# Kernel tuning notes

Measured on AMD Instinct MI355X. Metric: run time of the kernel, lower is better.

Reference implementation:

```python
import jax, jax.numpy as jnp
import numpy as np
from jax import lax

B, D, K = 65536, 256, 32  # batch, num_latent_dims, flow_depth


def setup_inputs() -> dict:
    key = jax.random.key(0)
    k1, k2, k3, k4, k5 = jax.random.split(key, 5)
    X = jax.random.normal(k1, (B, D), dtype=jnp.float32)
    h = jax.random.normal(k2, (B, D), dtype=jnp.float32)  # passed through, unused by planar math
    u = jax.random.normal(k3, (K, D), dtype=jnp.float32) * 0.1
    w = jax.random.normal(k4, (K, D), dtype=jnp.float32) * 0.1
    b = jax.random.normal(k5, (K,), dtype=jnp.float32) * 0.1
    return {"X": X, "h": h, "u": u, "w": w, "b": b}


def _planar_chain(z0, u, w, b):
    """Sequential planar normalizing flow: z_{k+1} = z_k + u_hat_k * tanh(w_k.z_k + b_k)."""

    def step(z, params):
        u_k, w_k, b_k = params  # (D,), (D,), scalar
        # enforce invertibility: u_hat so that w.u_hat >= -1
        wu = jnp.dot(w_k, u_k)
        u_hat = u_k + (jax.nn.softplus(wu) - 1.0 - wu) * w_k / jnp.dot(w_k, w_k)
        lin = z @ w_k + b_k              # (B,)
        t = jnp.tanh(lin)                # (B,)
        z_new = z + t[:, None] * u_hat[None, :]
        # psi = (1 - t^2) w ; log|det J| = log|1 + psi.u_hat|
        log_det = jnp.log(jnp.abs(1.0 + (1.0 - t * t) * jnp.dot(w_k, u_hat)) + 1e-8)
        return z_new, log_det

    z_final, log_dets = lax.scan(step, z0, (u, w, b))
    return z_final, log_dets  # (B, D), (K, B)


def reference(X, h, u, w, b):
    z = X.reshape(X.shape[0], X.shape[1])  # view(B, D, -1) then view(B, D) -> (B, D)
    z_final, log_det_jacobians = _planar_chain(z, u, w, b)
    return z_final, log_det_jacobians
```

## Files before the change

### kernel.cpp

```cpp
#include <hip/hip_runtime.h>


#define B_ 65536
#define D_ 256
#define K_ 32

__device__ float g_ws[17472];

__global__ __launch_bounds__(256) void nf_pre(const float* __restrict__ u_in,
                                              const float* __restrict__ w_in,
                                              const float* __restrict__ b_in) {
  __shared__ float wls[32 * 257];
  __shared__ float red[256];
  __shared__ float dots[128];
  __shared__ float coefk_s;
  const int t = threadIdx.x;
  const int myk = blockIdx.x;

  {
    const float4* wp = (const float4*)w_in;
#pragma unroll
    for (int j = 0; j < 8; ++j) {
      int idx = j * 256 + t;
      float4 v = wp[idx];
      int e = idx * 4;
      int k = e >> 8, d = e & 255;
      wls[k * 257 + d]     = v.x;
      wls[k * 257 + d + 1] = v.y;
      wls[k * 257 + d + 2] = v.z;
      wls[k * 257 + d + 3] = v.w;
    }
  }
  __syncthreads();

  {
    int id = t & 127, hh = t >> 7;
    int j = id & 31, typ = id >> 5;
    const float* A;
    const float* Bp;
    if (typ == 0)      { A = u_in + j * 256; Bp = wls + j * 257; }
    else if (typ == 1) { A = wls + j * 257;  Bp = wls + j * 257; }
    else if (typ == 2) { A = wls + j * 257;  Bp = wls + myk * 257; }
    else               { A = u_in + j * 256; Bp = wls + myk * 257; }
    float acc = 0.f;
    int d0 = hh * 128;
#pragma unroll 8
    for (int d = 0; d < 128; ++d) acc = fmaf(A[d0 + d], Bp[d0 + d], acc);
    red[t] = acc;
  }
  __syncthreads();
  if (t < 128) dots[t] = red[t] + red[t + 128];
  __syncthreads();

  float* wT = g_ws;
  float* uhatT = g_ws + 8192;
  float* Gt = g_ws + 16384;
  float* cs = g_ws + 17408;
  float* bfs = g_ws + 17440;

  if (t < 32) {
    float wu = dots[t], ww = dots[32 + t], wkw = dots[64 + t], ukw = dots[96 + t];
    float sp = fmaxf(wu, 0.f) + log1pf(__expf(-fabsf(wu)));
    float coef = (sp - 1.f - wu) / ww;
    Gt[myk * 32 + t] = fmaf(coef, wkw, ukw);
    if (t == myk) {
      cs[myk] = sp - 1.f;
      bfs[myk] = b_in[myk];
      coefk_s = coef;
    }
  }
  __syncthreads();
  {
    float coefk = coefk_s;
    float wv = wls[myk * 257 + t];
    float uhv = fmaf(coefk, wv, u_in[myk * 256 + t]);
    wT[t * 32 + myk] = wv;
    uhatT[t * 32 + myk] = uhv;
  }
}

__global__ __launch_bounds__(256) void nf_main(const float* __restrict__ X,
                                               float* __restrict__ out) {
  __shared__ float Xt[64 * 129];
  __shared__ float tls[128 * 33];

  const int t = threadIdx.x;
  const int lane = t & 63;
  const int r = ((t >> 7) << 6) | lane;
  const int half = __builtin_amdgcn_readfirstlane((t >> 6) & 1);
  const int hb = half * 32;
  const int row0 = blockIdx.x * 128;
  const size_t grow = (size_t)(row0 + r);
  const int r_ld = t >> 1, q = t & 1;

  const float* __restrict__ wT = g_ws;
  const float* __restrict__ uhatT = g_ws + 8192;
  const float* __restrict__ Gt = g_ws + 16384;
  const float* __restrict__ cs = g_ws + 17408;
  const float* __restrict__ bfs = g_ws + 17440;

  float4 pf[8];

  auto load_stage = [&](int s) {
    const float4* xp = (const float4*)X + (size_t)(row0 + r_ld) * 64 + s * 16 + q * 8;
#pragma unroll
    for (int j = 0; j < 8; ++j) pf[j] = xp[j];
  };
  auto store_stage = [&]() {
#pragma unroll
    for (int j = 0; j < 8; ++j) {
      int c0 = q * 32 + j * 4;
      Xt[(c0 + 0) * 129 + r_ld] = pf[j].x;
      Xt[(c0 + 1) * 129 + r_ld] = pf[j].y;
      Xt[(c0 + 2) * 129 + r_ld] = pf[j].z;
      Xt[(c0 + 3) * 129 + r_ld] = pf[j].w;
    }
  };

  float p[32];
#pragma unroll
  for (int k = 0; k < 32; ++k) p[k] = 0.f;

  load_stage(0);
  for (int s = 0; s < 4; ++s) {
    store_stage();
    __syncthreads();
    if (s < 3) load_stage(s + 1);
#pragma unroll
    for (int c = 0; c < 32; ++c) {
      float xc = Xt[(hb + c) * 129 + r];
      const float* wp = wT + (s * 64 + hb + c) * 32;
#pragma unroll
      for (int k = 0; k < 32; ++k) p[k] = fmaf(xc, wp[k], p[k]);
    }
    __syncthreads();
  }

  float* plds = Xt;
  if (half == 0) {
#pragma unroll
    for (int k = 0; k < 32; ++k) plds[r * 33 + k] = p[k];
  }
  load_stage(0);
  __syncthreads();

  float tv[32];
  if (half == 1) {
    float pfull[32];
#pragma unroll
    for (int k = 0; k < 32; ++k) pfull[k] = p[k] + plds[r * 33 + k] + bfs[k];
#pragma unroll
    for (int k = 0; k < 32; ++k) {
      float la = pfull[k], lb = 0.f;
      const float* gp = Gt + k * 32;
#pragma unroll
      for (int j = 0; j + 1 < k; j += 2) {
        la = fmaf(tv[j], gp[j], la);
        lb = fmaf(tv[j + 1], gp[j + 1], lb);
      }
      if (k & 1) la = fmaf(tv[k - 1], gp[k - 1], la);
      float lin = la + lb;
      float e = __expf(2.f * lin);
      float tk = 1.f - 2.f / (e + 1.f);
      tv[k] = tk;
      tls[r * 33 + k] = tk;
      float val = fabsf(fmaf(1.f - tk * tk, cs[k], 1.f)) + 1e-8f;
      out[(size_t)B_ * D_ + (size_t)k * B_ + grow] = __logf(val);
    }
  }
  __syncthreads();
#pragma unroll
  for (int k = 0; k < 32; ++k) tv[k] = tls[r * 33 + k];

  for (int s = 0; s < 4; ++s) {
    store_stage();
    __syncthreads();
    if (s < 3) load_stage(s + 1);
    float4 ov[8];
#pragma unroll
    for (int c2 = 0; c2 < 8; ++c2) {
      float zz[4];
#pragma unroll
      for (int m = 0; m < 4; ++m) {
        int cl = hb + c2 * 4 + m;
        float z0 = Xt[cl * 129 + r];
        const float* up = uhatT + (s * 64 + cl) * 32;
#pragma unroll
        for (int k = 0; k < 32; ++k) z0 = fmaf(tv[k], up[k], z0);
        zz[m] = z0;
      }
      ov[c2] = make_float4(zz[0], zz[1], zz[2], zz[3]);
    }
    float4* op = (float4*)(out + grow * 256 + s * 64 + hb);
#pragma unroll
    for (int c2 = 0; c2 < 8; ++c2) op[c2] = ov[c2];
    __syncthreads();
  }
}

extern "C" void kernel_launch(void* const* d_in, const int* in_sizes, int n_in,
                              void* d_out, int out_size, void* d_ws, size_t ws_size,
                              hipStream_t stream) {
  const float* X = (const float*)d_in[0];
  const float* u = (const float*)d_in[2];
  const float* w = (const float*)d_in[3];
  const float* b = (const float*)d_in[4];
  float* out = (float*)d_out;

  nf_pre<<<32, 256, 0, stream>>>(u, w, b);
  nf_main<<<B_ / 128, 256, 0, stream>>>(X, out);
}
```

Measured before the change: 241.2 us.

## Fuse parameter precompute into main kernel and use register-tiled outer-product GEMMs

Removes the separate preprocessing kernel: each block now recomputes u_hat, the Gram-like matrix G and the softplus coefficients from u, w and b in shared memory, then processes 256 rows instead of 128. Both the X·W projection and the t·u_hat update become 4x8 register-tiled outer products reading float4 from LDS, replacing per-thread 32-wide scalar loops over global/constant data. The aim is to save a launch and serialization and to raise arithmetic intensity per LDS load. In exchange every block redundantly does the small O(K²D) setup, and LDS use grows, which may lower occupancy.

```diff
diff --git a/kernel.cpp b/kernel.cpp
--- a/kernel.cpp
+++ b/kernel.cpp
@@ -4,196 +4,235 @@
 #define B_ 65536
 #define D_ 256
 #define K_ 32
-
-__device__ float g_ws[17472];
-
-__global__ __launch_bounds__(256) void nf_pre(const float* __restrict__ u_in,
-                                              const float* __restrict__ w_in,
-                                              const float* __restrict__ b_in) {
-  __shared__ float wls[32 * 257];
-  __shared__ float red[256];
-  __shared__ float dots[128];
-  __shared__ float coefk_s;
-  const int t = threadIdx.x;
-  const int myk = blockIdx.x;
-
-  {
-    const float4* wp = (const float4*)w_in;
-#pragma unroll
-    for (int j = 0; j < 8; ++j) {
-      int idx = j * 256 + t;
-      float4 v = wp[idx];
-      int e = idx * 4;
-      int k = e >> 8, d = e & 255;
-      wls[k * 257 + d]     = v.x;
-      wls[k * 257 + d + 1] = v.y;
-      wls[k * 257 + d + 2] = v.z;
-      wls[k * 257 + d + 3] = v.w;
-    }
-  }
-  __syncthreads();
-
-  {
-    int id = t & 127, hh = t >> 7;
-    int j = id & 31, typ = id >> 5;
-    const float* A;
-    const float* Bp;
-    if (typ == 0)      { A = u_in + j * 256; Bp = wls + j * 257; }
-    else if (typ == 1) { A = wls + j * 257;  Bp = wls + j * 257; }
-    else if (typ == 2) { A = wls + j * 257;  Bp = wls + myk * 257; }
-    else               { A = u_in + j * 256; Bp = wls + myk * 257; }
-    float acc = 0.f;
-    int d0 = hh * 128;
-#pragma unroll 8
-    for (int d = 0; d < 128; ++d) acc = fmaf(A[d0 + d], Bp[d0 + d], acc);
-    red[t] = acc;
-  }
-  __syncthreads();
-  if (t < 128) dots[t] = red[t] + red[t + 128];
-  __syncthreads();
-
-  float* wT = g_ws;
-  float* uhatT = g_ws + 8192;
-  float* Gt = g_ws + 16384;
-  float* cs = g_ws + 17408;
-  float* bfs = g_ws + 17440;
-
-  if (t < 32) {
-    float wu = dots[t], ww = dots[32 + t], wkw = dots[64 + t], ukw = dots[96 + t];
-    float sp = fmaxf(wu, 0.f) + log1pf(__expf(-fabsf(wu)));
-    float coef = (sp - 1.f - wu) / ww;
-    Gt[myk * 32 + t] = fmaf(coef, wkw, ukw);
-    if (t == myk) {
-      cs[myk] = sp - 1.f;
-      bfs[myk] = b_in[myk];
-      coefk_s = coef;
-    }
-  }
-  __syncthreads();
-  {
-    float coefk = coefk_s;
-    float wv = wls[myk * 257 + t];
-    float uhv = fmaf(coefk, wv, u_in[myk * 256 + t]);
-    wT[t * 32 + myk] = wv;
-    uhatT[t * 32 + myk] = uhv;
-  }
-}
-
-__global__ __launch_bounds__(256) void nf_main(const float* __restrict__ X,
-                                               float* __restrict__ out) {
-  __shared__ float Xt[64 * 129];
-  __shared__ float tls[128 * 33];
+#define ROWS 256
+#define XT_STRIDE 264
+#define UT_STRIDE 260
+
+__global__ __launch_bounds__(256) void nf_fused(const float* __restrict__ X,
+                                                const float* __restrict__ u_in,
+                                                const float* __restrict__ w_in,
+                                                const float* __restrict__ b_in,
+                                                float* __restrict__ out) {
+  __shared__ float wT1[8192];
+  __shared__ float uT2[32 * UT_STRIDE];
+  __shared__ float XtP[8448];
+  __shared__ float Gm[32 * 33];
+  __shared__ float cs_s[32], coefs_s[32], bfs_s[32];
 
   const int t = threadIdx.x;
   const int lane = t & 63;
-  const int r = ((t >> 7) << 6) | lane;
-  const int half = __builtin_amdgcn_readfirstlane((t >> 6) & 1);
-  const int hb = half * 32;
-  const int row0 = blockIdx.x * 128;
-  const size_t grow = (size_t)(row0 + r);
-  const int r_ld = t >> 1, q = t & 1;
-
-  const float* __restrict__ wT = g_ws;
-  const float* __restrict__ uhatT = g_ws + 8192;
-  const float* __restrict__ Gt = g_ws + 16384;
-  const float* __restrict__ cs = g_ws + 17408;
-  const float* __restrict__ bfs = g_ws + 17440;
+  const int wv = t >> 6;
+  const int rg = lane >> 2;
+  const int kq = lane & 3;
+  const int row0 = blockIdx.x * ROWS;
+  const int rp = t & 127;
+  const int ch = t >> 7;
+  const int xoff = wv * 64 + rg * 4;
+  const int kw = t >> 3;
+  const int d0g = (t & 7) * 32;
+
+  {
+    float4 tmp[8];
+    const float4* wp = (const float4*)(w_in + kw * 256 + d0g);
+#pragma unroll
+    for (int j = 0; j < 8; ++j) tmp[j] = wp[j];
+#pragma unroll
+    for (int j = 0; j < 8; ++j) {
+      wT1[(d0g + j * 4 + 0) * 32 + kw] = tmp[j].x;
+      wT1[(d0g + j * 4 + 1) * 32 + kw] = tmp[j].y;
+      wT1[(d0g + j * 4 + 2) * 32 + kw] = tmp[j].z;
+      wT1[(d0g + j * 4 + 3) * 32 + kw] = tmp[j].w;
+    }
+    const float4* up = (const float4*)(u_in + kw * 256 + d0g);
+#pragma unroll
+    for (int j = 0; j < 8; ++j) tmp[j] = up[j];
+    float4* ud = (float4*)&uT2[kw * UT_STRIDE + d0g];
+#pragma unroll
+    for (int j = 0; j < 8; ++j) ud[j] = tmp[j];
+    if (t < 32) bfs_s[t] = b_in[t];
+  }
 
   float4 pf[8];
-
+  const float* xbase = X + (size_t)(row0 + 2 * rp) * 256 + ch * 16;
   auto load_stage = [&](int s) {
-    const float4* xp = (const float4*)X + (size_t)(row0 + r_ld) * 64 + s * 16 + q * 8;
-#pragma unroll
-    for (int j = 0; j < 8; ++j) pf[j] = xp[j];
+    const float4* a = (const float4*)(xbase + s * 32);
+    const float4* b = (const float4*)(xbase + 256 + s * 32);
+#pragma unroll
+    for (int j = 0; j < 4; ++j) pf[j] = a[j];
+#pragma unroll
+    for (int j = 0; j < 4; ++j) pf[4 + j] = b[j];
   };
   auto store_stage = [&]() {
 #pragma unroll
+    for (int cc = 0; cc < 16; ++cc) {
+      const float* fa = (const float*)&pf[cc >> 2];
+      const float* fb = (const float*)&pf[4 + (cc >> 2)];
+      *(float2*)&XtP[(ch * 16 + cc) * XT_STRIDE + 2 * rp] =
+          make_float2(fa[cc & 3], fb[cc & 3]);
+    }
+  };
+  load_stage(0);
+  __syncthreads();
+
+  {
+    int qd = t >> 6, which = (t >> 5) & 1, j = t & 31;
+    int dlo = qd * 64;
+    float acc = 0.f;
+    if (which == 0) {
+#pragma unroll 8
+      for (int d = 0; d < 64; ++d)
+        acc = fmaf(wT1[(dlo + d) * 32 + j], uT2[j * UT_STRIDE + dlo + d], acc);
+    } else {
+#pragma unroll 8
+      for (int d = 0; d < 64; ++d) {
+        float wvv = wT1[(dlo + d) * 32 + j];
+        acc = fmaf(wvv, wvv, acc);
+      }
+    }
+    XtP[t] = acc;
+  }
+  __syncthreads();
+  if (t < 32) {
+    float wu = XtP[t] + XtP[64 + t] + XtP[128 + t] + XtP[192 + t];
+    float ww = XtP[32 + t] + XtP[96 + t] + XtP[160 + t] + XtP[224 + t];
+    float sp = fmaxf(wu, 0.f) + log1pf(__expf(-fabsf(wu)));
+    coefs_s[t] = (sp - 1.f - wu) / ww;
+    cs_s[t] = sp - 1.f;
+  }
+  __syncthreads();
+
+  {
+    float ck = coefs_s[kw];
+    float4* ud = (float4*)&uT2[kw * UT_STRIDE + d0g];
+#pragma unroll
     for (int j = 0; j < 8; ++j) {
-      int c0 = q * 32 + j * 4;
-      Xt[(c0 + 0) * 129 + r_ld] = pf[j].x;
-      Xt[(c0 + 1) * 129 + r_ld] = pf[j].y;
-      Xt[(c0 + 2) * 129 + r_ld] = pf[j].z;
-      Xt[(c0 + 3) * 129 + r_ld] = pf[j].w;
-    }
-  };
-
-  float p[32];
-#pragma unroll
-  for (int k = 0; k < 32; ++k) p[k] = 0.f;
-
+      float4 uvv = ud[j];
+      uvv.x = fmaf(ck, wT1[(d0g + j * 4 + 0) * 32 + kw], uvv.x);
+      uvv.y = fmaf(ck, wT1[(d0g + j * 4 + 1) * 32 + kw], uvv.y);
+      uvv.z = fmaf(ck, wT1[(d0g + j * 4 + 2) * 32 + kw], uvv.z);
+      uvv.w = fmaf(ck, wT1[(d0g + j * 4 + 3) * 32 + kw], uvv.w);
+      ud[j] = uvv;
+    }
+  }
+  __syncthreads();
+
+  {
+    int j = t & 31, kg = t >> 5;
+    float g0 = 0.f, g1 = 0.f, g2 = 0.f, g3 = 0.f;
+#pragma unroll 4
+    for (int d = 0; d < 256; ++d) {
+      float uj = uT2[j * UT_STRIDE + d];
+      g0 = fmaf(uj, wT1[d * 32 + kg], g0);
+      g1 = fmaf(uj, wT1[d * 32 + kg + 8], g1);
+      g2 = fmaf(uj, wT1[d * 32 + kg + 16], g2);
+      g3 = fmaf(uj, wT1[d * 32 + kg + 24], g3);
+    }
+    Gm[kg * 33 + j] = g0;
+    Gm[(kg + 8) * 33 + j] = g1;
+    Gm[(kg + 16) * 33 + j] = g2;
+    Gm[(kg + 24) * 33 + j] = g3;
+  }
+
+  float p[4][8];
+#pragma unroll
+  for (int a = 0; a < 4; ++a)
+#pragma unroll
+    for (int b2 = 0; b2 < 8; ++b2) p[a][b2] = 0.f;
+
+  for (int s = 0; s < 8; ++s) {
+    store_stage();
+    __syncthreads();
+    if (s < 7) load_stage(s + 1);
+#pragma unroll 8
+    for (int d = 0; d < 32; ++d) {
+      float4 xv = *(const float4*)&XtP[d * XT_STRIDE + xoff];
+      const float* wrow = &wT1[(s * 32 + d) * 32 + kq * 8];
+      float4 w0 = *(const float4*)wrow;
+      float4 w1 = *(const float4*)(wrow + 4);
+      const float xr[4] = {xv.x, xv.y, xv.z, xv.w};
+      const float wk[8] = {w0.x, w0.y, w0.z, w0.w, w1.x, w1.y, w1.z, w1.w};
+#pragma unroll
+      for (int a = 0; a < 4; ++a)
+#pragma unroll
+        for (int b2 = 0; b2 < 8; ++b2) p[a][b2] = fmaf(xr[a], wk[b2], p[a][b2]);
+    }
+    __syncthreads();
+  }
+
+#pragma unroll
+  for (int a = 0; a < 4; ++a) {
+    float4* dst = (float4*)&XtP[(xoff + a) * 32 + kq * 8];
+    dst[0] = make_float4(p[a][0], p[a][1], p[a][2], p[a][3]);
+    dst[1] = make_float4(p[a][4], p[a][5], p[a][6], p[a][7]);
+  }
+  __syncthreads();
   load_stage(0);
-  for (int s = 0; s < 4; ++s) {
-    store_stage();
-    __syncthreads();
-    if (s < 3) load_stage(s + 1);
-#pragma unroll
-    for (int c = 0; c < 32; ++c) {
-      float xc = Xt[(hb + c) * 129 + r];
-      const float* wp = wT + (s * 64 + hb + c) * 32;
-#pragma unroll
-      for (int k = 0; k < 32; ++k) p[k] = fmaf(xc, wp[k], p[k]);
-    }
-    __syncthreads();
-  }
-
-  float* plds = Xt;
-  if (half == 0) {
-#pragma unroll
-    for (int k = 0; k < 32; ++k) plds[r * 33 + k] = p[k];
-  }
-  load_stage(0);
-  __syncthreads();
-
-  float tv[32];
-  if (half == 1) {
+
+  {
     float pfull[32];
-#pragma unroll
-    for (int k = 0; k < 32; ++k) pfull[k] = p[k] + plds[r * 33 + k] + bfs[k];
+    const float4* ps = (const float4*)&XtP[t * 32];
+#pragma unroll
+    for (int j = 0; j < 8; ++j) {
+      float4 v = ps[j];
+      pfull[j * 4 + 0] = v.x + bfs_s[j * 4 + 0];
+      pfull[j * 4 + 1] = v.y + bfs_s[j * 4 + 1];
+      pfull[j * 4 + 2] = v.z + bfs_s[j * 4 + 2];
+      pfull[j * 4 + 3] = v.w + bfs_s[j * 4 + 3];
+    }
+    float tvv[32];
 #pragma unroll
     for (int k = 0; k < 32; ++k) {
       float la = pfull[k], lb = 0.f;
-      const float* gp = Gt + k * 32;
+      const float* gp = &Gm[k * 33];
 #pragma unroll
       for (int j = 0; j + 1 < k; j += 2) {
-        la = fmaf(tv[j], gp[j], la);
-        lb = fmaf(tv[j + 1], gp[j + 1], lb);
+        la = fmaf(tvv[j], gp[j], la);
+        lb = fmaf(tvv[j + 1], gp[j + 1], lb);
       }
-      if (k & 1) la = fmaf(tv[k - 1], gp[k - 1], la);
+      if (k & 1) la = fmaf(tvv[k - 1], gp[k - 1], la);
       float lin = la + lb;
       float e = __expf(2.f * lin);
       float tk = 1.f - 2.f / (e + 1.f);
-      tv[k] = tk;
-      tls[r * 33 + k] = tk;
-      float val = fabsf(fmaf(1.f - tk * tk, cs[k], 1.f)) + 1e-8f;
-      out[(size_t)B_ * D_ + (size_t)k * B_ + grow] = __logf(val);
-    }
-  }
-  __syncthreads();
-#pragma unroll
-  for (int k = 0; k < 32; ++k) tv[k] = tls[r * 33 + k];
-
-  for (int s = 0; s < 4; ++s) {
+      tvv[k] = tk;
+      wT1[k * 256 + t] = tk;
+      float val = fabsf(fmaf(1.f - tk * tk, cs_s[k], 1.f)) + 1e-8f;
+      out[(size_t)B_ * D_ + (size_t)k * B_ + row0 + t] = __logf(val);
+    }
+  }
+  __syncthreads();
+
+  for (int s = 0; s < 8; ++s) {
     store_stage();
     __syncthreads();
-    if (s < 3) load_stage(s + 1);
-    float4 ov[8];
-#pragma unroll
-    for (int c2 = 0; c2 < 8; ++c2) {
-      float zz[4];
-#pragma unroll
-      for (int m = 0; m < 4; ++m) {
-        int cl = hb + c2 * 4 + m;
-        float z0 = Xt[cl * 129 + r];
-        const float* up = uhatT + (s * 64 + cl) * 32;
-#pragma unroll
-        for (int k = 0; k < 32; ++k) z0 = fmaf(tv[k], up[k], z0);
-        zz[m] = z0;
-      }
-      ov[c2] = make_float4(zz[0], zz[1], zz[2], zz[3]);
-    }
-    float4* op = (float4*)(out + grow * 256 + s * 64 + hb);
-#pragma unroll
-    for (int c2 = 0; c2 < 8; ++c2) op[c2] = ov[c2];
+    if (s < 7) load_stage(s + 1);
+    float acc[4][8];
+#pragma unroll
+    for (int dd = 0; dd < 8; ++dd) {
+      float4 xv = *(const float4*)&XtP[(kq * 8 + dd) * XT_STRIDE + xoff];
+      acc[0][dd] = xv.x;
+      acc[1][dd] = xv.y;
+      acc[2][dd] = xv.z;
+      acc[3][dd] = xv.w;
+    }
+#pragma unroll 8
+    for (int k = 0; k < 32; ++k) {
+      float4 t4 = *(const float4*)&wT1[k * 256 + xoff];
+      const float* ur = &uT2[k * UT_STRIDE + s * 32 + kq * 8];
+      float4 u0 = *(const float4*)ur;
+      float4 u1 = *(const float4*)(ur + 4);
+      const float tr[4] = {t4.x, t4.y, t4.z, t4.w};
+      const float uk[8] = {u0.x, u0.y, u0.z, u0.w, u1.x, u1.y, u1.z, u1.w};
+#pragma unroll
+      for (int a = 0; a < 4; ++a)
+#pragma unroll
+        for (int b2 = 0; b2 < 8; ++b2) acc[a][b2] = fmaf(tr[a], uk[b2], acc[a][b2]);
+    }
+#pragma unroll
+    for (int a = 0; a < 4; ++a) {
+      float4* op = (float4*)(out + (size_t)(row0 + xoff + a) * 256 + s * 32 + kq * 8);
+      op[0] = make_float4(acc[a][0], acc[a][1], acc[a][2], acc[a][3]);
+      op[1] = make_float4(acc[a][4], acc[a][5], acc[a][6], acc[a][7]);
+    }
     __syncthreads();
   }
 }
@@ -207,6 +246,5 @@
   const float* b = (const float*)d_in[4];
   float* out = (float*)d_out;
 
-  nf_pre<<<32, 256, 0, stream>>>(u, w, b);
-  nf_main<<<B_ / 128, 256, 0, stream>>>(X, out);
+  nf_fused<<<B_ / ROWS, 256, 0, stream>>>(X, u, w, b, out);
 }
```

Result: faster. 209.4 us (-13.2%).
